# Optimization experiments

Hardware: AMD Instinct MI355X
Metric: run time of the kernel (lower is better)

The kernel has to match this reference:

```python
import jax, jax.numpy as jnp
import numpy as np

B, V, H, NT, K_CD = 4096, 1024, 1024, 2, 10
L1_REG, L2_REG = 1e-5, 1e-4


def setup_inputs() -> dict:
    key = jax.random.key(0)
    ks = jax.random.split(key, 10)
    v0 = jax.random.bernoulli(ks[0], 0.5, (B, V)).astype(jnp.float32)
    # two distinct non-trivial (non-Z) sites per sample, one in each half
    tau0 = jax.random.randint(ks[1], (B,), 0, V // 2)
    tau1 = V // 2 + jax.random.randint(ks[2], (B,), 0, V // 2)
    tau_idx = jnp.stack([tau0, tau1], axis=1).astype(jnp.int32)
    basis_choice = jax.random.randint(ks[3], (B, NT), 1, 3).astype(jnp.int32)  # X=1 or Y=2
    basis_ids = jnp.zeros((B, V), jnp.int32)
    basis_ids = basis_ids.at[jnp.arange(B)[:, None], tau_idx].set(basis_choice)
    s = 1.0 / np.sqrt(2.0)
    un = np.zeros((3, 2, 2, 2), np.float32)  # [basis, row, col, re/im]
    un[0, :, :, 0] = np.eye(2)                              # Z: identity
    un[1, :, :, 0] = s * np.array([[1, 1], [1, -1]])        # X: Hadamard
    un[2, :, :, 0] = s * np.array([[1, 0], [1, 0]])         # Y: K gate, real
    un[2, :, :, 1] = s * np.array([[0, -1], [0, 1]])        # Y: K gate, imag
    unitaries = jnp.asarray(un)
    weights_amp = jax.random.normal(ks[4], (H, V), jnp.float32) / np.sqrt(V)
    weights_phase = 0.01 * jax.random.normal(ks[5], (H, V), jnp.float32)
    visible_bias_amp = 0.01 * jax.random.normal(ks[6], (V,), jnp.float32)
    hidden_bias_amp = 0.01 * jax.random.normal(ks[7], (H,), jnp.float32)
    visible_bias_phase = 0.01 * jax.random.normal(ks[8], (V,), jnp.float32)
    hidden_bias_phase = 0.01 * jax.random.normal(ks[9], (H,), jnp.float32)
    return {"v0": v0, "basis_ids": basis_ids, "tau_idx": tau_idx, "unitaries": unitaries,
            "weights_amp": weights_amp, "visible_bias_amp": visible_bias_amp,
            "hidden_bias_amp": hidden_bias_amp, "weights_phase": weights_phase,
            "visible_bias_phase": visible_bias_phase, "hidden_bias_phase": hidden_bias_phase,
            "k": K_CD}


def _forward(v0, unitaries, weights_amp, visible_bias_amp, hidden_bias_amp,
             weights_phase, visible_bias_phase, hidden_bias_phase,
             basis_ids, tau_idx, k):
    Bsz, Vn = v0.shape
    NTn = tau_idx.shape[1]
    C = 2 ** NTn
    # all 2^NT assignments of the rotated (tau) sites -> [C, NT]
    S = jnp.asarray(np.array([[(c >> (NTn - 1 - t)) & 1 for t in range(NTn)]
                              for c in range(C)], np.int32))
    U = (unitaries[..., 0] + 1j * unitaries[..., 1]).astype(jnp.complex64)  # [3,2,2]
    b_tau = jnp.take_along_axis(basis_ids, tau_idx, axis=1)                 # [B,NT]
    v0_tau = jnp.take_along_axis(v0, tau_idx, axis=1).astype(jnp.int32)     # [B,NT]
    # product over tau sites of unitary elements U_b[v0_j, s_j] -> [B,C]
    Uelem = U[b_tau[:, None, :], v0_tau[:, None, :], S[None, :, :]]
    wU = jnp.prod(Uelem, axis=-1)
    # v' = v0 with tau sites replaced by each assignment s -> [B,C,V]
    onehot = jax.nn.one_hot(tau_idx, Vn, dtype=v0.dtype)                    # [B,NT,V]
    mask = onehot.sum(1)
    vp = v0[:, None, :] * (1.0 - mask[:, None, :]) \
         + jnp.einsum('btv,ct->bcv', onehot, S.astype(v0.dtype))
    # unnormalized wavefunction psi(v') = sqrt(p_amp(v')) * exp(i*log(p_phase(v'))/2)
    pre_amp = jnp.einsum('bcv,hv->bch', vp, weights_amp) + hidden_bias_amp
    pre_ph = jnp.einsum('bcv,hv->bch', vp, weights_phase) + hidden_bias_phase
    log_amp = 0.5 * (vp @ visible_bias_amp + jax.nn.softplus(pre_amp).sum(-1))  # [B,C]
    theta = 0.5 * (vp @ visible_bias_phase + jax.nn.softplus(pre_ph).sum(-1))
    # per-sample shift cancels exactly in A/B; keeps exp() in fp32 range
    log_amp = log_amp - jax.lax.stop_gradient(log_amp.max(axis=1, keepdims=True))
    psi = (jnp.exp(log_amp) * (jnp.cos(theta) + 1j * jnp.sin(theta))).astype(jnp.complex64)
    w = wU * psi                                   # [B,C] complex
    coef = w / w.sum(axis=1, keepdims=True)        # A/B weighting per sample
    sig_amp = jax.nn.sigmoid(pre_amp)
    sig_ph = jax.nn.sigmoid(pre_ph)
    inv_b = 1.0 / Bsz
    Lw_amp = jnp.einsum('bc,bch,bcv->hv', coef, sig_amp, vp) * inv_b
    Lw_ph = jnp.einsum('bc,bch,bcv->hv', coef, sig_ph, vp) * inv_b
    Lvb = jnp.einsum('bc,bcv->v', coef, vp) * inv_b
    Lhb_amp = jnp.einsum('bc,bch->h', coef, sig_amp) * inv_b
    Lhb_ph = jnp.einsum('bc,bch->h', coef, sig_ph) * inv_b
    # amplitude params take Re(L) (negated positive phase); phase params take Im(L)
    g_w_amp = -jnp.real(Lw_amp)
    g_vb_amp = -jnp.real(Lvb)
    g_hb_amp = -jnp.real(Lhb_amp)
    g_w_ph = jnp.imag(Lw_ph)
    g_vb_ph = jnp.imag(Lvb)
    g_hb_ph = jnp.imag(Lhb_ph)
    # ---- CD-k Gibbs negative phase (amplitude RBM only) ----
    base_key = jax.random.key(1234)
    def gibbs_step(i, v):
        kh = jax.random.fold_in(base_key, 2 * i)
        kv = jax.random.fold_in(base_key, 2 * i + 1)
        ph = jax.nn.sigmoid(v @ weights_amp.T + hidden_bias_amp)
        h = (jax.random.uniform(kh, ph.shape) < ph).astype(v.dtype)
        pv = jax.nn.sigmoid(h @ weights_amp + visible_bias_amp)
        return (jax.random.uniform(kv, pv.shape) < pv).astype(v.dtype)
    vk = jax.lax.stop_gradient(jax.lax.fori_loop(0, k, gibbs_step, v0))
    sig_k = jax.nn.sigmoid(vk @ weights_amp.T + hidden_bias_amp)
    g_w_amp = g_w_amp + jnp.einsum('bh,bv->hv', sig_k, vk) * inv_b
    g_vb_amp = g_vb_amp + vk.mean(0)
    g_hb_amp = g_hb_amp + sig_k.mean(0)
    # ---- L1/L2 regularization on weight gradients ----
    g_w_amp = g_w_amp + L2_REG * weights_amp + L1_REG * jnp.sign(weights_amp)
    g_w_ph = g_w_ph + L2_REG * weights_phase + L1_REG * jnp.sign(weights_phase)
    return (g_w_amp, g_vb_amp, g_hb_amp, g_w_ph, g_vb_ph, g_hb_ph)


def reference(v0, basis_ids, tau_idx, unitaries, weights_amp, visible_bias_amp,
              hidden_bias_amp, weights_phase, visible_bias_phase, hidden_bias_phase, k):
    return _forward(v0, unitaries, weights_amp, visible_bias_amp, hidden_bias_amp,
                    weights_phase, visible_bias_phase, hidden_bias_phase,
                    basis_ids, tau_idx, k)
```

## Files before the change

### kernel.cpp

```cpp
#include <hip/hip_runtime.h>
#include <cstdint>
#include <cstddef>

#define BSZ 4096
#define VN  1024
#define HN  1024
#define NSTEPS 10

static constexpr float INVB = 1.0f / 4096.0f;
static constexpr float L1R  = 1e-5f;
static constexpr float L2R  = 1e-4f;

typedef __attribute__((ext_vector_type(8)))  __bf16        bf16x8;
typedef __attribute__((ext_vector_type(8)))  unsigned short ushort8;
typedef __attribute__((ext_vector_type(4)))  unsigned short ushort4v;
typedef __attribute__((ext_vector_type(4)))  float          f32x4;
typedef __attribute__((ext_vector_type(16))) float          f32x16;

__device__ static inline unsigned short f2bf(float x){
  unsigned u = __float_as_uint(x);
  unsigned r = (u + 0x7FFFu + ((u >> 16) & 1u)) >> 16;
  return (unsigned short)r;
}
__device__ static inline float bf2f(unsigned short s){
  return __uint_as_float(((unsigned)s) << 16);
}

__device__ __forceinline__ void gload16(const void* g, void* l){
  __builtin_amdgcn_global_load_lds(
      (__attribute__((address_space(1))) void*)(g),
      (__attribute__((address_space(3))) void*)(l),
      16, 0, 0);
}

#define TFR(x0,x1,r) { x0 += x1; x1 = ((x1)<<(r))|((x1)>>(32-(r))); x1 ^= x0; }

__host__ __device__ static inline void tf2x32(unsigned k0, unsigned k1,
                                              unsigned x0, unsigned x1,
                                              unsigned &o0, unsigned &o1)
{
  const unsigned ks2 = k0 ^ k1 ^ 0x1BD11BDAu;
  x0 += k0; x1 += k1;
  TFR(x0,x1,13) TFR(x0,x1,15) TFR(x0,x1,26) TFR(x0,x1,6)
  x0 += k1; x1 += ks2 + 1u;
  TFR(x0,x1,17) TFR(x0,x1,29) TFR(x0,x1,16) TFR(x0,x1,24)
  x0 += ks2; x1 += k0 + 2u;
  TFR(x0,x1,13) TFR(x0,x1,15) TFR(x0,x1,26) TFR(x0,x1,6)
  x0 += k0; x1 += k1 + 3u;
  TFR(x0,x1,17) TFR(x0,x1,29) TFR(x0,x1,16) TFR(x0,x1,24)
  x0 += k1; x1 += ks2 + 4u;
  TFR(x0,x1,13) TFR(x0,x1,15) TFR(x0,x1,26) TFR(x0,x1,6)
  x0 += ks2; x1 += k0 + 5u;
  o0 = x0; o1 = x1;
}

__device__ static inline float tf_uniform(unsigned k0, unsigned k1, unsigned e)
{
  unsigned o0, o1; tf2x32(k0, k1, 0u, e, o0, o1);
  const unsigned r = o0 ^ o1;
  return __uint_as_float((r >> 9) | 0x3f800000u) - 1.0f;
}

__device__ static inline float sigmoidf(float x){ return 1.0f/(1.0f+expf(-x)); }

__global__ void zero_kernel(float* __restrict__ p, int n){
  int i = blockIdx.x*256 + threadIdx.x;
  if (i < n) p[i] = 0.0f;
}

__global__ void prep_kernel(const float* __restrict__ v0,
                            const int* __restrict__ tau,
                            float* __restrict__ v0m,
                            float* __restrict__ v_cur,
                            unsigned short* __restrict__ v0m_bf,
                            unsigned short* __restrict__ v_bf)
{
  int i = blockIdx.x*256 + threadIdx.x;
  int b = i >> 10;
  int v = i & (VN-1);
  float x = v0[i];
  v_cur[i] = x;
  v_bf[i]  = f2bf(x);
  int t0 = tau[2*b], t1 = tau[2*b+1];
  float xm = (v==t0 || v==t1) ? 0.0f : x;
  v0m[i]    = xm;
  v0m_bf[i] = f2bf(xm);
}

__global__ void transpose_kernel(const float* __restrict__ Wa,
                                 const float* __restrict__ Wp,
                                 float* __restrict__ WTa,
                                 float* __restrict__ WTp)
{
  __shared__ float tile[32][33];
  const float* in = blockIdx.z ? Wp : Wa;
  float* out      = blockIdx.z ? WTp : WTa;
  int x  = blockIdx.x*32 + threadIdx.x;
  int y0 = blockIdx.y*32;
  for (int j = threadIdx.y; j < 32; j += 8)
    tile[j][threadIdx.x] = in[(size_t)(y0+j)*VN + x];
  __syncthreads();
  int xo  = y0 + threadIdx.x;
  int yo0 = blockIdx.x*32;
  for (int j = threadIdx.y; j < 32; j += 8)
    out[(size_t)(yo0+j)*HN + xo] = tile[threadIdx.x][j];
}

__global__ void transpose_to_bf(const float* __restrict__ X,
                                unsigned short* __restrict__ XT,
                                float* __restrict__ cs)
{
  __shared__ float tile[32][33];
  const int tx = threadIdx.x, ty = threadIdx.y;
  int x  = blockIdx.x*32 + tx;
  int y0 = blockIdx.y*32;
  for (int j = ty; j < 32; j += 8)
    tile[j][tx] = X[(size_t)(y0+j)*1024 + x];
  __syncthreads();
  int xo  = y0 + tx;
  int yo0 = blockIdx.x*32;
  for (int j = ty; j < 32; j += 8)
    XT[(size_t)(yo0+j)*BSZ + xo] = f2bf(tile[tx][j]);
  float s = tile[ty][tx] + tile[ty+8][tx] + tile[ty+16][tx] + tile[ty+24][tx];
  __syncthreads();
  tile[ty][tx] = s;
  __syncthreads();
  if (ty == 0){
    float t = 0.f;
    #pragma unroll
    for (int j = 0; j < 8; j++) t += tile[j][tx];
    atomicAdd(cs + x, t);
  }
}

__global__ void split_weights(const float* __restrict__ Wa,
                              const float* __restrict__ Wp,
                              const float* __restrict__ WTa,
                              const float* __restrict__ WTp,
                              unsigned short* __restrict__ WaHi,
                              unsigned short* __restrict__ WaLo,
                              unsigned short* __restrict__ WpHi,
                              unsigned short* __restrict__ WpLo,
                              unsigned short* __restrict__ WaTHi,
                              unsigned short* __restrict__ WaTLo,
                              unsigned short* __restrict__ WpTHi)
{
  size_t i = (size_t)blockIdx.x*256 + threadIdx.x;
  float w = Wa[i];  unsigned short h = f2bf(w);
  WaHi[i] = h;  WaLo[i] = f2bf(w - bf2f(h));
  w = Wp[i];  h = f2bf(w);
  WpHi[i] = h;  WpLo[i] = f2bf(w - bf2f(h));
  w = WTa[i]; h = f2bf(w);
  WaTHi[i] = h; WaTLo[i] = f2bf(w - bf2f(h));
  WpTHi[i] = f2bf(WTp[i]);
}

#define GM 64
#define GN 64
#define GK 64

template<int MODE>
__global__ __launch_bounds__(256) void mfma_nt(
    const unsigned short* __restrict__ A,
    const unsigned short* __restrict__ Bhi,
    const unsigned short* __restrict__ Blo,
    const float* __restrict__ bias,
    unsigned short* __restrict__ out_bf,
    float* __restrict__ out_f,
    unsigned key0, unsigned key1)
{
  constexpr int K = 1024;
  constexpr int N = 1024;
  __shared__ ushort8 ldsA [GM*8];
  __shared__ ushort8 ldsBh[GN*8];
  __shared__ ushort8 ldsBl[GN*8];

  const int orig = blockIdx.x + gridDim.x * blockIdx.y;
  const int swz  = (orig & 7) * 128 + (orig >> 3);
  const int bx   = swz & 15, by = swz >> 4;
  const int m0   = by*GM, n0 = bx*GN;

  const int tid  = threadIdx.x;
  const int lane = tid & 63, w = tid >> 6;
  const int wm = w >> 1, wn = w & 1;
  const int l31 = lane & 31, hi = lane >> 5;
  const int rsub = lane >> 3;
  const int cch  = lane & 7;

  f32x16 acc = {};

  const int arow = wm*32 + l31;
  const int brow = wn*32 + l31;
  const int aswz = arow & 7;
  const int bswz = brow & 7;
  const int aidx = arow*8;
  const int bidx = brow*8;

  for (int kt = 0; kt < K/GK; ++kt){
    __syncthreads();
    const size_t kbase = (size_t)kt*GK;
    #pragma unroll
    for (int p = 0; p < 2; p++){
      const int row  = p*32 + w*8 + rsub;
      const int csrc = cch ^ (row & 7);
      gload16(A   + (size_t)(m0+row)*K + kbase + csrc*8, &ldsA [(p*32 + w*8)*8]);
      gload16(Bhi + (size_t)(n0+row)*K + kbase + csrc*8, &ldsBh[(p*32 + w*8)*8]);
      gload16(Blo + (size_t)(n0+row)*K + kbase + csrc*8, &ldsBl[(p*32 + w*8)*8]);
    }
    __syncthreads();

    #pragma unroll
    for (int s = 0; s < 4; s++){
      const int c = s*2 + hi;
      const bf16x8 a  = __builtin_bit_cast(bf16x8, ldsA [aidx + (c ^ aswz)]);
      const bf16x8 bh = __builtin_bit_cast(bf16x8, ldsBh[bidx + (c ^ bswz)]);
      const bf16x8 bl = __builtin_bit_cast(bf16x8, ldsBl[bidx + (c ^ bswz)]);
      acc = __builtin_amdgcn_mfma_f32_32x32x16_bf16(a, bh, acc, 0, 0, 0);
      acc = __builtin_amdgcn_mfma_f32_32x32x16_bf16(a, bl, acc, 0, 0, 0);
    }
  }

  const int n  = n0 + wn*32 + l31;
  const float bv = bias[n];
  const int mbase = m0 + wm*32 + 4*hi;
  #pragma unroll
  for (int r = 0; r < 16; r++){
    const int m = mbase + (r&3) + 8*(r>>2);
    const float pre = acc[r] + bv;
    const size_t o = (size_t)m*N + n;
    if constexpr (MODE == 0 || MODE == 1){
      const float p = sigmoidf(pre);
      const float u = tf_uniform(key0, key1, (unsigned)(m*N + n));
      out_bf[o] = (u < p) ? (unsigned short)0x3F80 : (unsigned short)0;
      if constexpr (MODE == 1) out_f[o] = (u < p) ? 1.0f : 0.0f;
    } else if constexpr (MODE == 2){
      out_f[o] = sigmoidf(pre);
    } else {
      out_f[o]  = pre;
      out_bf[o] = f2bf(pre);
    }
  }
}

template<int NPROD>
__global__ __launch_bounds__(256) void mfma_grad(
    const unsigned short* __restrict__ A1,
    const unsigned short* __restrict__ B1,
    const unsigned short* __restrict__ A2,
    const unsigned short* __restrict__ B2,
    const float* __restrict__ Wreg,
    float* __restrict__ gW)
{
  constexpr int K = BSZ;
  __shared__ ushort8 lA1[64*8];
  __shared__ ushort8 lB1[64*8];
  __shared__ ushort8 lA2[(NPROD==2)?64*8:1];
  __shared__ ushort8 lB2[(NPROD==2)?64*8:1];

  const int tid  = threadIdx.x;
  const int m0   = blockIdx.y*64, n0 = blockIdx.x*64;
  const int lane = tid & 63, w = tid >> 6;
  const int wm = w >> 1, wn = w & 1;
  const int l31 = lane & 31, hi = lane >> 5;
  const int srow = tid >> 3, sc = tid & 7;

  f32x16 acc1a = {}, acc1b = {}, acc2a = {}, acc2b = {};

  const int arow = wm*32 + l31;
  const int brow = wn*32 + l31;
  const int aswz = arow & 7, bswz = brow & 7;
  const int aidx = arow*8,  bidx = brow*8;

  for (int kt = 0; kt < K/64; ++kt){
    __syncthreads();
    const size_t kof = (size_t)kt*64 + sc*8;
    #pragma unroll
    for (int p = 0; p < 2; p++){
      const int row = p*32 + srow;
      const int c = sc ^ (row & 7);
      lA1[row*8 + c] = *(const ushort8*)(A1 + (size_t)(m0+row)*K + kof);
      lB1[row*8 + c] = *(const ushort8*)(B1 + (size_t)(n0+row)*K + kof);
      if constexpr (NPROD==2){
        lA2[row*8 + c] = *(const ushort8*)(A2 + (size_t)(m0+row)*K + kof);
        lB2[row*8 + c] = *(const ushort8*)(B2 + (size_t)(n0+row)*K + kof);
      }
    }
    __syncthreads();
    #pragma unroll
    for (int s = 0; s < 4; s++){
      const int c = s*2 + hi;
      const bf16x8 a1 = __builtin_bit_cast(bf16x8, lA1[aidx + (c ^ aswz)]);
      const bf16x8 b1 = __builtin_bit_cast(bf16x8, lB1[bidx + (c ^ bswz)]);
      if (s & 1) acc1b = __builtin_amdgcn_mfma_f32_32x32x16_bf16(a1, b1, acc1b, 0,0,0);
      else       acc1a = __builtin_amdgcn_mfma_f32_32x32x16_bf16(a1, b1, acc1a, 0,0,0);
      if constexpr (NPROD==2){
        const bf16x8 a2 = __builtin_bit_cast(bf16x8, lA2[aidx + (c ^ aswz)]);
        const bf16x8 b2 = __builtin_bit_cast(bf16x8, lB2[bidx + (c ^ bswz)]);
        if (s & 1) acc2b = __builtin_amdgcn_mfma_f32_32x32x16_bf16(a2, b2, acc2b, 0,0,0);
        else       acc2a = __builtin_amdgcn_mfma_f32_32x32x16_bf16(a2, b2, acc2a, 0,0,0);
      }
    }
  }

  const int n = n0 + wn*32 + l31;
  #pragma unroll
  for (int r = 0; r < 16; r++){
    const int m = m0 + wm*32 + 4*hi + (r&3) + 8*(r>>2);
    const size_t o = (size_t)m*VN + n;
    float val;
    if constexpr (NPROD==2)
      val = INVB*((acc1a[r]+acc1b[r]) - (acc2a[r]+acc2b[r]));
    else
      val = INVB*(acc1a[r]+acc1b[r]);
    const float wv = Wreg[o];
    const float sg = (wv>0.f)?1.f:((wv<0.f)?-1.f:0.f);
    gW[o] += val + L2R*wv + L1R*sg;
  }
}

__global__ __launch_bounds__(256) void coef_ramp_kernel(
    const float* __restrict__ pre0a, const float* __restrict__ pre0p,
    const float* __restrict__ WTa,   const float* __restrict__ WTp,
    const float* __restrict__ v0,
    const float* __restrict__ vbA,   const float* __restrict__ vbP,
    const int*   __restrict__ tau,   const int*   __restrict__ basis,
    const float* __restrict__ unit,
    float* __restrict__ coefRe, float* __restrict__ coefIm,
    float* __restrict__ tmpA,   float* __restrict__ tmpP,
    float* __restrict__ Ramp,   float* __restrict__ Iph)
{
  const int b = blockIdx.x;
  const int t = threadIdx.x;
  const int t0 = tau[2*b], t1 = tau[2*b+1];

  float d[6] = {0,0,0,0,0,0};
  float st_sa[4], st_sp[4], st_a0[4], st_a1[4], st_p0[4], st_p1[4];

  #pragma unroll
  for (int i = 0; i < 4; i++){
    const int h = t + i*256;
    const float pa = pre0a[(size_t)b*HN + h], pp = pre0p[(size_t)b*HN + h];
    const float a0 = WTa[(size_t)t0*HN + h], a1 = WTa[(size_t)t1*HN + h];
    const float p0 = WTp[(size_t)t0*HN + h], p1 = WTp[(size_t)t1*HN + h];
    const float sa  = sigmoidf(pa);
    const float sp  = sigmoidf(pp);
    const float s1a = sa*(1.f-sa), ta2 = 1.f-2.f*sa, s2a = s1a*ta2;
    const float s1p = sp*(1.f-sp), tp2 = 1.f-2.f*sp, s2p = s1p*tp2;
    const float a01 = a0 + a1, p01 = p0 + p1;
    d[0] += a1 *(sa + a1 *(0.5f*s1a + 0.16666667f*a1 *s2a));
    d[1] += a0 *(sa + a0 *(0.5f*s1a + 0.16666667f*a0 *s2a));
    d[2] += a01*(sa + a01*(0.5f*s1a + 0.16666667f*a01*s2a));
    d[3] += p1 *(sp + p1 *(0.5f*s1p + 0.16666667f*p1 *s2p));
    d[4] += p0 *(sp + p0 *(0.5f*s1p + 0.16666667f*p0 *s2p));
    d[5] += p01*(sp + p01*(0.5f*s1p + 0.16666667f*p01*s2p));
    st_sa[i]=sa; st_sp[i]=sp; st_a0[i]=a0; st_a1[i]=a1; st_p0[i]=p0; st_p1[i]=p1;
  }

  __shared__ float red[6][4];
  __shared__ float lcr[4], lci[4];
  const int lane = t & 63, wv = t >> 6;
  #pragma unroll
  for (int i=0;i<6;i++){
    float x = d[i];
    for (int off=32; off>0; off>>=1) x += __shfl_down(x, off);
    if (lane==0) red[i][wv] = x;
  }
  __syncthreads();

  if (t==0){
    double ds[6];
    #pragma unroll
    for (int i=0;i<6;i++)
      ds[i] = (double)red[i][0]+red[i][1]+red[i][2]+red[i][3];

    const int bas0 = basis[(size_t)b*VN + t0], bas1 = basis[(size_t)b*VN + t1];
    const int x0 = (int)v0[(size_t)b*VN + t0], x1 = (int)v0[(size_t)b*VN + t1];
    const double A0 = vbA[t0], A1 = vbA[t1], P0 = vbP[t0], P1 = vbP[t1];

    double la[4], th[4];
    la[0]=0.0;                th[0]=0.0;
    la[1]=0.5*(A1+ds[0]);     th[1]=0.5*(P1+ds[3]);
    la[2]=0.5*(A0+ds[1]);     th[2]=0.5*(P0+ds[4]);
    la[3]=0.5*(A0+A1+ds[2]);  th[3]=0.5*(P0+P1+ds[5]);

    double wR[4], wI[4], sr=0.0, si=0.0;
    #pragma unroll
    for (int c=0;c<4;c++){
      const int s0 = (c>>1)&1, s1 = c&1;
      const float* u0 = unit + (((size_t)bas0*2 + x0)*2 + s0)*2;
      const float* u1 = unit + (((size_t)bas1*2 + x1)*2 + s1)*2;
      const double uR = (double)u0[0]*u1[0] - (double)u0[1]*u1[1];
      const double uI = (double)u0[0]*u1[1] + (double)u0[1]*u1[0];
      const double e  = exp(la[c]);
      const double cs = cos(th[c]), sn = sin(th[c]);
      wR[c] = e*(uR*cs - uI*sn);
      wI[c] = e*(uR*sn + uI*cs);
      sr += wR[c]; si += wI[c];
    }
    const double dd = sr*sr + si*si;
    #pragma unroll
    for (int c=0;c<4;c++){
      const float cr = (float)((wR[c]*sr + wI[c]*si)/dd);
      const float ci = (float)((wI[c]*sr - wR[c]*si)/dd);
      coefRe[b*4+c] = cr;  coefIm[b*4+c] = ci;
      lcr[c] = cr;         lci[c] = ci;
    }
    atomicAdd(tmpA + t0, lcr[2]+lcr[3]);
    atomicAdd(tmpA + t1, lcr[1]+lcr[3]);
    atomicAdd(tmpP + t0, lci[2]+lci[3]);
    atomicAdd(tmpP + t1, lci[1]+lci[3]);
  }
  __syncthreads();

  const float cr0=lcr[0], cr1=lcr[1], cr2=lcr[2], cr3=lcr[3];
  const float ci0=lci[0], ci1=lci[1], ci2=lci[2], ci3=lci[3];

  #pragma unroll
  for (int i = 0; i < 4; i++){
    const int h = t + i*256;
    const float sa = st_sa[i], sp = st_sp[i];
    const float a0 = st_a0[i], a1 = st_a1[i], p0 = st_p0[i], p1 = st_p1[i];
    const float s1a = sa*(1.f-sa), ta2 = 1.f-2.f*sa;
    const float s2a = s1a*ta2,     s3a = s1a*(ta2*ta2 - 2.f*s1a);
    const float s1p = sp*(1.f-sp), tp2 = 1.f-2.f*sp;
    const float s2p = s1p*tp2,     s3p = s1p*(tp2*tp2 - 2.f*s1p);
    const float a01 = a0 + a1, p01 = p0 + p1;
    const float sgA1 = sa + a1 *(s1a + a1 *(0.5f*s2a + 0.16666667f*a1 *s3a));
    const float sgA0 = sa + a0 *(s1a + a0 *(0.5f*s2a + 0.16666667f*a0 *s3a));
    const float sgA01= sa + a01*(s1a + a01*(0.5f*s2a + 0.16666667f*a01*s3a));
    const float sgP1 = sp + p1 *(s1p + p1 *(0.5f*s2p + 0.16666667f*p1 *s3p));
    const float sgP0 = sp + p0 *(s1p + p0 *(0.5f*s2p + 0.16666667f*p0 *s3p));
    const float sgP01= sp + p01*(s1p + p01*(0.5f*s2p + 0.16666667f*p01*s3p));
    Ramp[(size_t)b*HN + h] = cr0*sa + cr1*sgA1 + cr2*sgA0 + cr3*sgA01;
    Iph [(size_t)b*HN + h] = ci0*sp + ci1*sgP1 + ci2*sgP0 + ci3*sgP01;
  }
}

__global__ void csr_count(const int* __restrict__ tau, int* __restrict__ cnt){
  int b = blockIdx.x*256 + threadIdx.x;
  atomicAdd(cnt + tau[2*b],   1);
  atomicAdd(cnt + tau[2*b+1], 1);
}

__global__ __launch_bounds__(1024) void csr_scan(const int* __restrict__ cnt,
                                                 int* __restrict__ off,
                                                 int* __restrict__ cur){
  __shared__ int s[1024];
  const int t = threadIdx.x;
  s[t] = cnt[t];
  __syncthreads();
  for (int d=1; d<1024; d<<=1){
    int v = 0;
    if (t >= d) v = s[t-d];
    __syncthreads();
    s[t] += v;
    __syncthreads();
  }
  const int excl = (t==0) ? 0 : s[t-1];
  off[t] = excl; cur[t] = excl;
}

__global__ void csr_fill(const int* __restrict__ tau, int* __restrict__ cur,
                         int* __restrict__ list){
  int b = blockIdx.x*256 + threadIdx.x;
  int p0 = atomicAdd(cur + tau[2*b],   1); list[p0] = b;
  int p1 = atomicAdd(cur + tau[2*b+1], 1); list[p1] = b;
}

__global__ __launch_bounds__(256) void scatter_v3(
    const unsigned short* __restrict__ pre0aBF,
    const unsigned short* __restrict__ pre0pBF,
    const unsigned short* __restrict__ WaTHi,
    const unsigned short* __restrict__ WpTHi,
    const int*   __restrict__ tau,
    const float* __restrict__ coefRe, const float* __restrict__ coefIm,
    const int* __restrict__ cnt, const int* __restrict__ off,
    const int* __restrict__ list,
    float* __restrict__ gSa, float* __restrict__ gSp)
{
  const int v  = blockIdx.x;
  const int h0 = threadIdx.x * 4;
  const int n  = cnt[v];
  const int o  = off[v];
  const int c_lo = (v < 512) ? 2 : 1;
  const bool lo_half = (v < 512);

  float accA[4] = {0,0,0,0}, accP[4] = {0,0,0,0};
  if (n > 0){
    const ushort4v avu = *(const ushort4v*)(WaTHi + (size_t)v*HN + h0);
    const ushort4v pvu = *(const ushort4v*)(WpTHi + (size_t)v*HN + h0);
    float av[4], pv[4];
    #pragma unroll
    for (int j=0;j<4;j++){ av[j]=bf2f(avu[j]); pv[j]=bf2f(pvu[j]); }
    for (int e = o; e < o + n; e++){
      const int b  = list[e];
      const int ot = lo_half ? tau[2*b+1] : tau[2*b];
      const ushort4v ao = *(const ushort4v*)(WaTHi  + (size_t)ot*HN + h0);
      const ushort4v po = *(const ushort4v*)(WpTHi  + (size_t)ot*HN + h0);
      const ushort4v pa = *(const ushort4v*)(pre0aBF + (size_t)b*HN + h0);
      const ushort4v pp = *(const ushort4v*)(pre0pBF + (size_t)b*HN + h0);
      const float crl = coefRe[b*4 + c_lo], cr3 = coefRe[b*4 + 3];
      const float cil = coefIm[b*4 + c_lo], ci3 = coefIm[b*4 + 3];
      #pragma unroll
      for (int j=0;j<4;j++){
        const float paf = bf2f(pa[j]) + av[j];
        const float ppf = bf2f(pp[j]) + pv[j];
        accA[j] += crl*sigmoidf(paf) + cr3*sigmoidf(paf + bf2f(ao[j]));
        accP[j] += cil*sigmoidf(ppf) + ci3*sigmoidf(ppf + bf2f(po[j]));
      }
    }
  }
  f32x4 ra, rp;
  #pragma unroll
  for (int j=0;j<4;j++){ ra[j]=accA[j]; rp[j]=accP[j]; }
  *(f32x4*)(gSa + (size_t)v*HN + h0) = ra;
  *(f32x4*)(gSp + (size_t)v*HN + h0) = rp;
}

__global__ void tadd_kernel(const float* __restrict__ gSa,
                            const float* __restrict__ gSp,
                            float* __restrict__ gWa,
                            float* __restrict__ gWp)
{
  __shared__ float ta[32][33], tp[32][33];
  const int tx = threadIdx.x, ty = threadIdx.y;
  const int v0 = blockIdx.x*32, h0 = blockIdx.y*32;
  for (int j = ty; j < 32; j += 8){
    ta[j][tx] = gSa[(size_t)(v0+j)*HN + h0 + tx];
    tp[j][tx] = gSp[(size_t)(v0+j)*HN + h0 + tx];
  }
  __syncthreads();
  for (int j = ty; j < 32; j += 8){
    gWa[(size_t)(h0+j)*VN + v0 + tx] = -INVB*ta[tx][j];
    gWp[(size_t)(h0+j)*VN + v0 + tx] =  INVB*tp[tx][j];
  }
}

__global__ void final_small(
    const float* __restrict__ csV0m, const float* __restrict__ csVk,
    const float* __restrict__ csSigk, const float* __restrict__ csRamp,
    const float* __restrict__ csIph,
    const float* __restrict__ tmpA, const float* __restrict__ tmpP,
    float* __restrict__ gVa, float* __restrict__ gHa,
    float* __restrict__ gVp, float* __restrict__ gHp)
{
  const int j = blockIdx.x*256 + threadIdx.x;
  if (j < VN){
    gVa[j] = INVB*(csVk[j] - csV0m[j] - tmpA[j]);
    gVp[j] = INVB*tmpP[j];
  }
  if (j < HN){
    gHa[j] = INVB*(csSigk[j] - csRamp[j]);
    gHp[j] = INVB*csIph[j];
  }
}

extern "C" void kernel_launch(void* const* d_in, const int* in_sizes, int n_in,
                              void* d_out, int out_size, void* d_ws, size_t ws_size,
                              hipStream_t stream)
{
  const float* v0    = (const float*)d_in[0];
  const int*   basis = (const int*)  d_in[1];
  const int*   tau   = (const int*)  d_in[2];
  const float* unit  = (const float*)d_in[3];
  const float* Wa    = (const float*)d_in[4];
  const float* vbA   = (const float*)d_in[5];
  const float* hbA   = (const float*)d_in[6];
  const float* Wp    = (const float*)d_in[7];
  const float* vbP   = (const float*)d_in[8];
  const float* hbP   = (const float*)d_in[9];

  float* ws    = (float*)d_ws;
  float* v0m   = ws;  ws += (size_t)BSZ*VN;
  float* v_cur = ws;  ws += (size_t)BSZ*VN;
  float* h_buf = ws;  ws += (size_t)BSZ*HN;
  float* WTa   = ws;  ws += (size_t)VN*HN;
  float* WTp   = ws;  ws += (size_t)VN*HN;
  float* pre0a = ws;  ws += (size_t)BSZ*HN;
  float* pre0p = ws;  ws += (size_t)BSZ*HN;
  float* Ramp  = ws;  ws += (size_t)BSZ*HN;
  float* Iph   = ws;  ws += (size_t)BSZ*HN;
  float* coefRe= ws;  ws += (size_t)BSZ*4;
  float* coefIm= ws;  ws += (size_t)BSZ*4;
  float* tmpA  = ws;  ws += VN;
  float* tmpP  = ws;  ws += VN;
  float* csV0m = ws;  ws += VN;
  float* csVk  = ws;  ws += VN;
  float* csSigk= ws;  ws += HN;
  float* csRamp= ws;  ws += HN;
  float* csIph = ws;  ws += HN;
  int*   csrCnt = (int*)ws;  ws += VN;
  int*   csrOff = (int*)ws;  ws += VN;
  int*   csrCur = (int*)ws;  ws += VN;
  int*   csrLst = (int*)ws;  ws += 2*BSZ;
  unsigned short* v_bf    = (unsigned short*)ws;  ws += (size_t)BSZ*VN/2;
  unsigned short* h_bf    = (unsigned short*)ws;  ws += (size_t)BSZ*HN/2;
  unsigned short* v0m_bf  = (unsigned short*)ws;  ws += (size_t)BSZ*VN/2;
  unsigned short* WaHi    = (unsigned short*)ws;  ws += (size_t)HN*VN/2;
  unsigned short* WaLo    = (unsigned short*)ws;  ws += (size_t)HN*VN/2;
  unsigned short* WpHi    = (unsigned short*)ws;  ws += (size_t)HN*VN/2;
  unsigned short* WpLo    = (unsigned short*)ws;  ws += (size_t)HN*VN/2;
  unsigned short* WaTHi   = (unsigned short*)ws;  ws += (size_t)HN*VN/2;
  unsigned short* WaTLo   = (unsigned short*)ws;  ws += (size_t)HN*VN/2;
  unsigned short* WpTHi   = (unsigned short*)ws;  ws += (size_t)HN*VN/2;

  float* sig_k = h_buf;
  unsigned short* pre0aBF = (unsigned short*)h_buf;
  unsigned short* pre0pBF = pre0aBF + (size_t)BSZ*HN;
  float* gSa = pre0a;
  float* gSp = pre0a + (size_t)VN*HN;
  unsigned short* v0mT  = (unsigned short*)pre0a;
  unsigned short* vkT   = v0mT + (size_t)VN*BSZ;
  unsigned short* RampT = (unsigned short*)pre0p;
  unsigned short* IphT  = RampT + (size_t)HN*BSZ;
  unsigned short* sigkT = (unsigned short*)WTa;

  float* out = (float*)d_out;
  float* gWa = out;
  float* gVa = gWa + (size_t)HN*VN;
  float* gHa = gVa + VN;
  float* gWp = gHa + HN;
  float* gVp = gWp + (size_t)HN*VN;
  float* gHp = gVp + VN;

  const dim3 gemm_grid(VN/GN, BSZ/GM);
  const dim3 tr_grid(1024/32, BSZ/32);
  const dim3 tr_blk(32, 8);

  zero_kernel<<<dim3(40), 256, 0, stream>>>(tmpA, 10*1024);
  prep_kernel<<<dim3(BSZ*VN/256), 256, 0, stream>>>(v0, tau, v0m, v_cur, v0m_bf, v_bf);
  transpose_kernel<<<dim3(VN/32, HN/32, 2), dim3(32,8), 0, stream>>>(Wa, Wp, WTa, WTp);
  split_weights<<<dim3(HN*VN/256), 256, 0, stream>>>(
      Wa, Wp, WTa, WTp, WaHi, WaLo, WpHi, WpLo, WaTHi, WaTLo, WpTHi);

  mfma_nt<3><<<gemm_grid, 256, 0, stream>>>(
      v0m_bf, WaHi, WaLo, hbA, pre0aBF, pre0a, 0u, 0u);
  mfma_nt<3><<<gemm_grid, 256, 0, stream>>>(
      v0m_bf, WpHi, WpLo, hbP, pre0pBF, pre0p, 0u, 0u);
  coef_ramp_kernel<<<dim3(BSZ), 256, 0, stream>>>(
      pre0a, pre0p, WTa, WTp, v0, vbA, vbP, tau, basis, unit,
      coefRe, coefIm, tmpA, tmpP, Ramp, Iph);

  csr_count<<<dim3(BSZ/256), 256, 0, stream>>>(tau, csrCnt);
  csr_scan <<<dim3(1), 1024, 0, stream>>>(csrCnt, csrOff, csrCur);
  csr_fill <<<dim3(BSZ/256), 256, 0, stream>>>(tau, csrCur, csrLst);
  scatter_v3<<<dim3(VN), 256, 0, stream>>>(
      pre0aBF, pre0pBF, WaTHi, WpTHi, tau, coefRe, coefIm,
      csrCnt, csrOff, csrLst, gSa, gSp);
  tadd_kernel<<<dim3(VN/32, HN/32), dim3(32,8), 0, stream>>>(
      gSa, gSp, gWa, gWp);

  for (int i = 0; i < NSTEPS; i++){
    unsigned kh0, kh1, kv0, kv1;
    tf2x32(0u, 1234u, 0u, (unsigned)(2*i),   kh0, kh1);
    tf2x32(0u, 1234u, 0u, (unsigned)(2*i+1), kv0, kv1);
    mfma_nt<0><<<gemm_grid, 256, 0, stream>>>(
        v_bf, WaHi, WaLo, hbA, h_bf, nullptr, kh0, kh1);
    if (i < NSTEPS-1)
      mfma_nt<0><<<gemm_grid, 256, 0, stream>>>(
          h_bf, WaTHi, WaTLo, vbA, v_bf, nullptr, kv0, kv1);
    else
      mfma_nt<1><<<gemm_grid, 256, 0, stream>>>(
          h_bf, WaTHi, WaTLo, vbA, v_bf, v_cur, kv0, kv1);
  }
  mfma_nt<2><<<gemm_grid, 256, 0, stream>>>(
      v_bf, WaHi, WaLo, hbA, nullptr, sig_k, 0u, 0u);

  transpose_to_bf<<<tr_grid, tr_blk, 0, stream>>>(v0m,   v0mT,  csV0m);
  transpose_to_bf<<<tr_grid, tr_blk, 0, stream>>>(v_cur, vkT,   csVk);
  transpose_to_bf<<<tr_grid, tr_blk, 0, stream>>>(Ramp,  RampT, csRamp);
  transpose_to_bf<<<tr_grid, tr_blk, 0, stream>>>(Iph,   IphT,  csIph);
  transpose_to_bf<<<tr_grid, tr_blk, 0, stream>>>(sig_k, sigkT, csSigk);

  mfma_grad<2><<<dim3(VN/64, HN/64), 256, 0, stream>>>(
      sigkT, vkT, RampT, v0mT, Wa, gWa);
  mfma_grad<1><<<dim3(VN/64, HN/64), 256, 0, stream>>>(
      IphT, v0mT, nullptr, nullptr, Wp, gWp);

  final_small<<<dim3(4), 256, 0, stream>>>(
      csV0m, csVk, csSigk, csRamp, csIph, tmpA, tmpP, gVa, gHa, gVp, gHp);
}
```

Before: 935.8 us.

## Split-K the weight-gradient GEMMs with partial buffers and a finalize kernel

Splits the K=4096 reduction of the two weight-gradient GEMMs into four chunks along grid z, which raises the block count from 256 to 1024 so more of the GPU's compute units are occupied. Each chunk writes fp32 partials into reused scratch buffers. A new elementwise kernel sums the partials and applies the scaling and L1/L2 regularization. Tile loads now go through gload16, which looks like a direct global-to-LDS load helper. The cost is extra partial-buffer traffic, one more launch, and a dependence on v0m and v_cur being dead at this point.

```diff
diff --git a/kernel.cpp b/kernel.cpp
--- a/kernel.cpp
+++ b/kernel.cpp
@@ -243,13 +243,12 @@
 }
 
 template<int NPROD>
-__global__ __launch_bounds__(256) void mfma_grad(
+__global__ __launch_bounds__(256) void mfma_grad_split(
     const unsigned short* __restrict__ A1,
     const unsigned short* __restrict__ B1,
     const unsigned short* __restrict__ A2,
     const unsigned short* __restrict__ B2,
-    const float* __restrict__ Wreg,
-    float* __restrict__ gW)
+    float* __restrict__ part)
 {
   constexpr int K = BSZ;
   __shared__ ushort8 lA1[64*8];
@@ -259,10 +258,12 @@
 
   const int tid  = threadIdx.x;
   const int m0   = blockIdx.y*64, n0 = blockIdx.x*64;
+  const int kz   = blockIdx.z;
   const int lane = tid & 63, w = tid >> 6;
   const int wm = w >> 1, wn = w & 1;
   const int l31 = lane & 31, hi = lane >> 5;
-  const int srow = tid >> 3, sc = tid & 7;
+  const int rsub = lane >> 3;
+  const int cch  = lane & 7;
 
   f32x16 acc1a = {}, acc1b = {}, acc2a = {}, acc2b = {};
 
@@ -271,18 +272,18 @@
   const int aswz = arow & 7, bswz = brow & 7;
   const int aidx = arow*8,  bidx = brow*8;
 
-  for (int kt = 0; kt < K/64; ++kt){
+  for (int kt = 0; kt < 16; ++kt){
     __syncthreads();
-    const size_t kof = (size_t)kt*64 + sc*8;
+    const size_t kbase = (size_t)kz*1024 + (size_t)kt*64;
     #pragma unroll
     for (int p = 0; p < 2; p++){
-      const int row = p*32 + srow;
-      const int c = sc ^ (row & 7);
-      lA1[row*8 + c] = *(const ushort8*)(A1 + (size_t)(m0+row)*K + kof);
-      lB1[row*8 + c] = *(const ushort8*)(B1 + (size_t)(n0+row)*K + kof);
+      const int row  = p*32 + w*8 + rsub;
+      const int csrc = cch ^ (row & 7);
+      gload16(A1 + (size_t)(m0+row)*K + kbase + csrc*8, &lA1[(p*32 + w*8)*8]);
+      gload16(B1 + (size_t)(n0+row)*K + kbase + csrc*8, &lB1[(p*32 + w*8)*8]);
       if constexpr (NPROD==2){
-        lA2[row*8 + c] = *(const ushort8*)(A2 + (size_t)(m0+row)*K + kof);
-        lB2[row*8 + c] = *(const ushort8*)(B2 + (size_t)(n0+row)*K + kof);
+        gload16(A2 + (size_t)(m0+row)*K + kbase + csrc*8, &lA2[(p*32 + w*8)*8]);
+        gload16(B2 + (size_t)(n0+row)*K + kbase + csrc*8, &lB2[(p*32 + w*8)*8]);
       }
     }
     __syncthreads();
@@ -302,20 +303,33 @@
     }
   }
 
+  float* outp = part + (size_t)kz * HN * VN;
   const int n = n0 + wn*32 + l31;
   #pragma unroll
   for (int r = 0; r < 16; r++){
     const int m = m0 + wm*32 + 4*hi + (r&3) + 8*(r>>2);
     const size_t o = (size_t)m*VN + n;
-    float val;
     if constexpr (NPROD==2)
-      val = INVB*((acc1a[r]+acc1b[r]) - (acc2a[r]+acc2b[r]));
+      outp[o] = (acc1a[r]+acc1b[r]) - (acc2a[r]+acc2b[r]);
     else
-      val = INVB*(acc1a[r]+acc1b[r]);
-    const float wv = Wreg[o];
-    const float sg = (wv>0.f)?1.f:((wv<0.f)?-1.f:0.f);
-    gW[o] += val + L2R*wv + L1R*sg;
-  }
+      outp[o] = acc1a[r]+acc1b[r];
+  }
+}
+
+__global__ __launch_bounds__(256) void finalize_grad(
+    const float* __restrict__ partA, const float* __restrict__ partP,
+    const float* __restrict__ Wa,    const float* __restrict__ Wp,
+    float* __restrict__ gWa, float* __restrict__ gWp)
+{
+  const size_t i  = (size_t)blockIdx.x*256 + threadIdx.x;
+  const size_t MN = (size_t)HN*VN;
+  const float sA = ((partA[i] + partA[MN+i]) + partA[2*MN+i]) + partA[3*MN+i];
+  const float sP = ((partP[i] + partP[MN+i]) + partP[2*MN+i]) + partP[3*MN+i];
+  const float wa = Wa[i], wp = Wp[i];
+  const float sga = (wa>0.f)?1.f:((wa<0.f)?-1.f:0.f);
+  const float sgp = (wp>0.f)?1.f:((wp<0.f)?-1.f:0.f);
+  gWa[i] += INVB*sA + L2R*wa + L1R*sga;
+  gWp[i] += INVB*sP + L2R*wp + L1R*sgp;
 }
 
 __global__ __launch_bounds__(256) void coef_ramp_kernel(
@@ -614,6 +628,8 @@
   unsigned short* RampT = (unsigned short*)pre0p;
   unsigned short* IphT  = RampT + (size_t)HN*BSZ;
   unsigned short* sigkT = (unsigned short*)WTa;
+  float* partA = v0m;
+  float* partP = v_cur;
 
   float* out = (float*)d_out;
   float* gWa = out;
@@ -672,10 +688,12 @@
   transpose_to_bf<<<tr_grid, tr_blk, 0, stream>>>(Iph,   IphT,  csIph);
   transpose_to_bf<<<tr_grid, tr_blk, 0, stream>>>(sig_k, sigkT, csSigk);
 
-  mfma_grad<2><<<dim3(VN/64, HN/64), 256, 0, stream>>>(
-      sigkT, vkT, RampT, v0mT, Wa, gWa);
-  mfma_grad<1><<<dim3(VN/64, HN/64), 256, 0, stream>>>(
-      IphT, v0mT, nullptr, nullptr, Wp, gWp);
+  mfma_grad_split<2><<<dim3(VN/64, HN/64, 4), 256, 0, stream>>>(
+      sigkT, vkT, RampT, v0mT, partA);
+  mfma_grad_split<1><<<dim3(VN/64, HN/64, 4), 256, 0, stream>>>(
+      IphT, v0mT, nullptr, nullptr, partP);
+  finalize_grad<<<dim3(HN*VN/256), 256, 0, stream>>>(
+      partA, partP, Wa, Wp, gWa, gWp);
 
   final_small<<<dim3(4), 256, 0, stream>>>(
       csV0m, csVk, csSigk, csRamp, csIph, tmpA, tmpP, gVa, gHa, gVp, gHp);
```

After: 895.3 us. 1.05x faster.
